# Kernel optimization log

Hardware: AMD Instinct MI355X
Metric: run time of the kernel (lower is better)

The kernel has to match this reference:

```python
import jax, jax.numpy as jnp
import numpy as np

N, K, C = 10000, 64, 128


def setup_inputs() -> dict:
    key = jax.random.key(0)
    ks = jax.random.split(key, 6)
    return {
        "real": jax.random.normal(ks[0], (N, C), dtype=jnp.float32),
        "imag": jax.random.normal(ks[1], (N, C), dtype=jnp.float32),
        "Qreal": jax.random.normal(ks[2], (N, K), dtype=jnp.float32) / np.sqrt(N),
        "Qimag": jax.random.normal(ks[3], (N, K), dtype=jnp.float32) / np.sqrt(N),
        "Ritz": jax.random.uniform(ks[4], (K,), dtype=jnp.float32),
        "weight": jax.random.normal(ks[5], (C, C), dtype=jnp.float32) * np.sqrt(2.0 / (C + C)),  # xavier-ish scale
        "long_diff": 5,
    }


def reference(real, imag, Qreal, Qimag, Ritz, weight, long_diff):
    # TT = Ritz ** long_diff ; spectral filters L = Q diag(TT) Q^H split into real/imag
    TT = jnp.power(Ritz, long_diff)  # [K]
    QrT = Qreal * TT  # [N,K] columns scaled by TT (== Qreal @ diag(TT))
    QiT = Qimag * TT
    L_real = QrT @ Qreal.T + QiT @ Qimag.T  # [N,N]
    L_imag = QiT @ Qreal.T - QrT @ Qimag.T  # [N,N]
    # complex spmm + shared dense weight: (L @ X_complex) @ W
    res_real = (L_real @ real - L_imag @ imag) @ weight  # [N,C]
    res_imag = (L_imag @ real + L_real @ imag) @ weight  # [N,C]
    # complex ReLU: mask by sign of real part
    mask = (res_real >= 0).astype(res_real.dtype)
    return real + mask * res_real, imag + mask * res_imag
```

## Files before the change

kernel.cpp:

```cpp
#include <hip/hip_runtime.h>

#define NN 10000
#define KK 64
#define CC 128
#define OUTOFF (NN * CC)
#define NA 256
#define CHUNKS_A 625

__device__ __forceinline__ float4 f4fma(float s, float4 v, float4 a) {
    a.x = fmaf(s, v.x, a.x); a.y = fmaf(s, v.y, a.y);
    a.z = fmaf(s, v.z, a.z); a.w = fmaf(s, v.w, a.w);
    return a;
}
__device__ __forceinline__ float4 f4add(float4 a, float4 b) {
    a.x += b.x; a.y += b.y; a.z += b.z; a.w += b.w; return a;
}


__global__ __launch_bounds__(512) void kA(const float* __restrict__ re,
                                          const float* __restrict__ im,
                                          const float* __restrict__ Qr,
                                          const float* __restrict__ Qi,
                                          float* __restrict__ part)
{
    __shared__ float4 smem[1536];
    const int t = threadIdx.x;
    const int bid = blockIdx.x;
    const int kt = t & 15;
    const int ctA = t >> 4;
    const int row_q = (t & 255) >> 4, q_q = t & 15;
    const int row_x = t >> 5,          q_x = t & 31;
    const float4* gq  = (const float4*)((t < 256) ? Qr : Qi);
    const float4* gre = (const float4*)re;
    const float4* gim = (const float4*)im;

    float aU[4][4] = {}, aV[4][4] = {};

    int cb = bid;
    float4 r0 = gq [(size_t)(cb * 16 + row_q) * 16 + q_q];
    float4 r1 = gre[(size_t)(cb * 16 + row_x) * 32 + q_x];
    float4 r2 = gim[(size_t)(cb * 16 + row_x) * 32 + q_x];

    while (true) {
        smem[t] = r0; smem[512 + t] = r1; smem[1024 + t] = r2;
        __syncthreads();
        const int nx = cb + NA;
        if (nx < CHUNKS_A) {
            const int m0 = nx * 16;
            r0 = gq [(size_t)(m0 + row_q) * 16 + q_q];
            r1 = gre[(size_t)(m0 + row_x) * 32 + q_x];
            r2 = gim[(size_t)(m0 + row_x) * 32 + q_x];
        }
#pragma unroll 4
        for (int rr = 0; rr < 16; ++rr) {
            float4 q_r = smem[rr * 16 + kt];
            float4 q_i = smem[256 + rr * 16 + kt];
            float4 x_r = smem[512 + rr * 32 + ctA];
            float4 x_i = smem[1024 + rr * 32 + ctA];
            float qr_[4] = {q_r.x, q_r.y, q_r.z, q_r.w};
            float qi_[4] = {q_i.x, q_i.y, q_i.z, q_i.w};
            float xr_[4] = {x_r.x, x_r.y, x_r.z, x_r.w};
            float xi_[4] = {x_i.x, x_i.y, x_i.z, x_i.w};
#pragma unroll
            for (int a = 0; a < 4; ++a)
#pragma unroll
                for (int b = 0; b < 4; ++b) {
                    aU[a][b] = fmaf(qr_[a], xr_[b], aU[a][b]);
                    aU[a][b] = fmaf(qi_[a], xi_[b], aU[a][b]);
                    aV[a][b] = fmaf(qi_[a], xr_[b], aV[a][b]);
                    aV[a][b] = fmaf(-qr_[a], xi_[b], aV[a][b]);
                }
        }
        __syncthreads();
        if (nx >= CHUNKS_A) break;
        cb = nx;
    }
    float* base = part + (size_t)bid * 16384;
    const int k0 = kt * 4, c0 = ctA * 4;
#pragma unroll
    for (int a = 0; a < 4; ++a) {
        *(float4*)(base + (k0 + a) * CC + c0)        = make_float4(aU[a][0], aU[a][1], aU[a][2], aU[a][3]);
        *(float4*)(base + 8192 + (k0 + a) * CC + c0) = make_float4(aV[a][0], aV[a][1], aV[a][2], aV[a][3]);
    }
}

__global__ __launch_bounds__(256) void kRB(const float* __restrict__ part,
                                           const float* __restrict__ Ritz,
                                           const int* __restrict__ ldp,
                                           const float* __restrict__ W,
                                           float* __restrict__ UVW)
{
    __shared__ float4 red4[256];
    __shared__ float rowS[128];
    const int t = threadIdx.x;
    const int m = blockIdx.x >> 6, k = blockIdx.x & 63;
    const int q = t & 31, sl = t >> 5;

    const float4* p = (const float4*)part + (size_t)sl * 4096 + m * 2048 + k * 32 + q;
    float4 z = make_float4(0.f, 0.f, 0.f, 0.f);
    float4 s0 = z, s1 = z, s2 = z, s3 = z;
#pragma unroll 2
    for (int jj = 0; jj < 8; ++jj) {
        s0 = f4add(s0, p[0]);
        s1 = f4add(s1, p[(size_t)8  * 4096]);
        s2 = f4add(s2, p[(size_t)16 * 4096]);
        s3 = f4add(s3, p[(size_t)24 * 4096]);
        p += (size_t)32 * 4096;
    }
    red4[t] = f4add(f4add(s0, s1), f4add(s2, s3));
    __syncthreads();
    if (t < 32) {
        float4 tot = z;
#pragma unroll
        for (int g = 0; g < 8; ++g) tot = f4add(tot, red4[g * 32 + t]);
        ((float4*)rowS)[t] = tot;
    }
    __syncthreads();
    if (t < 128) {
        float acc = 0.f;
#pragma unroll 8
        for (int cp = 0; cp < 128; ++cp)
            acc = fmaf(rowS[cp], W[cp * 128 + t], acc);
        const int ld = *ldp;
        const float rz = Ritz[k];
        float tt = 1.f;
        for (int i = 0; i < ld; ++i) tt *= rz;
        UVW[m * 8192 + k * 128 + t] = tt * acc;
    }
}

__global__ __launch_bounds__(256) void kC(const float* __restrict__ re,
                                          const float* __restrict__ im,
                                          const float* __restrict__ Qr,
                                          const float* __restrict__ Qi,
                                          const float* __restrict__ UVW,
                                          float* __restrict__ out)
{
    __shared__ float4 s[4096];
    const int t = threadIdx.x;
    {
        const float4* g = (const float4*)UVW;
        for (int i = t; i < 4096; i += 256) s[i] = g[i];
    }
    __syncthreads();
    const int ct = t & 31;
    const int r  = t >> 5;
    const int na = blockIdx.x * 16 + r;
    const int nb = na + 8;

    const float4* qra = (const float4*)(Qr + (size_t)na * KK);
    const float4* qia = (const float4*)(Qi + (size_t)na * KK);
    const float4* qrb = (const float4*)(Qr + (size_t)nb * KK);
    const float4* qib = (const float4*)(Qi + (size_t)nb * KK);

    float4 z = make_float4(0.f, 0.f, 0.f, 0.f);
    float4 Ra = z, Ia = z, Rb = z, Ib = z;

#pragma unroll 4
    for (int k4 = 0; k4 < 16; ++k4) {
        float4 QRa = qra[k4], QIa = qia[k4];
        float4 QRb = qrb[k4], QIb = qib[k4];
        float ar[4] = {QRa.x, QRa.y, QRa.z, QRa.w};
        float ai[4] = {QIa.x, QIa.y, QIa.z, QIa.w};
        float br[4] = {QRb.x, QRb.y, QRb.z, QRb.w};
        float bi[4] = {QIb.x, QIb.y, QIb.z, QIb.w};
#pragma unroll
        for (int j = 0; j < 4; ++j) {
            const int k = k4 * 4 + j;
            float4 uw = s[k * 32 + ct];
            float4 vw = s[2048 + k * 32 + ct];
            Ra = f4fma(ar[j], uw, Ra); Ra = f4fma(ai[j], vw, Ra);
            Ia = f4fma(ai[j], uw, Ia); Ia = f4fma(-ar[j], vw, Ia);
            Rb = f4fma(br[j], uw, Rb); Rb = f4fma(bi[j], vw, Rb);
            Ib = f4fma(bi[j], uw, Ib); Ib = f4fma(-br[j], vw, Ib);
        }
    }
    const int cc = ct * 4;
    {
        float4 rin = *(const float4*)(re + (size_t)na * CC + cc);
        float4 iin = *(const float4*)(im + (size_t)na * CC + cc);
        float4 orr, oii;
        orr.x = rin.x + (Ra.x >= 0.f ? Ra.x : 0.f); oii.x = iin.x + (Ra.x >= 0.f ? Ia.x : 0.f);
        orr.y = rin.y + (Ra.y >= 0.f ? Ra.y : 0.f); oii.y = iin.y + (Ra.y >= 0.f ? Ia.y : 0.f);
        orr.z = rin.z + (Ra.z >= 0.f ? Ra.z : 0.f); oii.z = iin.z + (Ra.z >= 0.f ? Ia.z : 0.f);
        orr.w = rin.w + (Ra.w >= 0.f ? Ra.w : 0.f); oii.w = iin.w + (Ra.w >= 0.f ? Ia.w : 0.f);
        *(float4*)(out + (size_t)na * CC + cc)          = orr;
        *(float4*)(out + OUTOFF + (size_t)na * CC + cc) = oii;
    }
    {
        float4 rin = *(const float4*)(re + (size_t)nb * CC + cc);
        float4 iin = *(const float4*)(im + (size_t)nb * CC + cc);
        float4 orr, oii;
        orr.x = rin.x + (Rb.x >= 0.f ? Rb.x : 0.f); oii.x = iin.x + (Rb.x >= 0.f ? Ib.x : 0.f);
        orr.y = rin.y + (Rb.y >= 0.f ? Rb.y : 0.f); oii.y = iin.y + (Rb.y >= 0.f ? Ib.y : 0.f);
        orr.z = rin.z + (Rb.z >= 0.f ? Rb.z : 0.f); oii.z = iin.z + (Rb.z >= 0.f ? Ib.z : 0.f);
        orr.w = rin.w + (Rb.w >= 0.f ? Rb.w : 0.f); oii.w = iin.w + (Rb.w >= 0.f ? Ib.w : 0.f);
        *(float4*)(out + (size_t)nb * CC + cc)          = orr;
        *(float4*)(out + OUTOFF + (size_t)nb * CC + cc) = oii;
    }
}

extern "C" void kernel_launch(void* const* d_in, const int* in_sizes, int n_in,
                              void* d_out, int out_size, void* d_ws, size_t ws_size,
                              hipStream_t stream) {
    const float* re   = (const float*)d_in[0];
    const float* im   = (const float*)d_in[1];
    const float* Qr   = (const float*)d_in[2];
    const float* Qi   = (const float*)d_in[3];
    const float* Ritz = (const float*)d_in[4];
    const float* W    = (const float*)d_in[5];
    const int*   ldp  = (const int*)d_in[6];
    float* out = (float*)d_out;
    float* ws  = (float*)d_ws;

    float* part = ws;
    float* UVW  = ws + (size_t)NA * 16384;

    kA <<<NA,  512, 0, stream>>>(re, im, Qr, Qi, part);
    kRB<<<128, 256, 0, stream>>>(part, Ritz, ldp, W, UVW);
    kC <<<625, 256, 0, stream>>>(re, im, Qr, Qi, UVW, out);
}
```

Baseline: 114.3 us.

## Fuse partial-sum reduction into first kernel via atomic ticket and grid spin-wait

The separate reduction kernel is merged into the first kernel. Each block takes an atomic ticket after writing its partials, and the last 128 ticket holders spin until all 256 blocks finish, then do the reduction plus weight multiply. This removes one kernel launch and its boundary gap, but adds a memset launch and relies on all 256 blocks being co-resident so the spin-wait cannot deadlock. The output kernel also moves to 512-thread blocks covering 32 rows each, with a tail guard.

After: 125.5 us. 9.8% more time.

```diff
diff --git a/kernel.cpp b/kernel.cpp
--- a/kernel.cpp
+++ b/kernel.cpp
@@ -6,6 +6,10 @@
 #define OUTOFF (NN * CC)
 #define NA 256
 #define CHUNKS_A 625
+#define NRED 128
+
+#define UVW_OFF ((size_t)NA * 16384)
+#define CNT_OFF (UVW_OFF + 16384)
 
 __device__ __forceinline__ float4 f4fma(float s, float4 v, float4 a) {
     a.x = fmaf(s, v.x, a.x); a.y = fmaf(s, v.y, a.y);
@@ -16,120 +20,135 @@
     a.x += b.x; a.y += b.y; a.z += b.z; a.w += b.w; return a;
 }
 
-
-__global__ __launch_bounds__(512) void kA(const float* __restrict__ re,
-                                          const float* __restrict__ im,
-                                          const float* __restrict__ Qr,
-                                          const float* __restrict__ Qi,
-                                          float* __restrict__ part)
+__global__ __launch_bounds__(512) void kAR(const float* __restrict__ re,
+                                           const float* __restrict__ im,
+                                           const float* __restrict__ Qr,
+                                           const float* __restrict__ Qi,
+                                           const float* __restrict__ Ritz,
+                                           const float* __restrict__ W,
+                                           const int* __restrict__ ldp,
+                                           float* __restrict__ ws)
 {
     __shared__ float4 smem[1536];
+    __shared__ int ticketS;
     const int t = threadIdx.x;
     const int bid = blockIdx.x;
-    const int kt = t & 15;
-    const int ctA = t >> 4;
-    const int row_q = (t & 255) >> 4, q_q = t & 15;
-    const int row_x = t >> 5,          q_x = t & 31;
-    const float4* gq  = (const float4*)((t < 256) ? Qr : Qi);
-    const float4* gre = (const float4*)re;
-    const float4* gim = (const float4*)im;
-
-    float aU[4][4] = {}, aV[4][4] = {};
-
-    int cb = bid;
-    float4 r0 = gq [(size_t)(cb * 16 + row_q) * 16 + q_q];
-    float4 r1 = gre[(size_t)(cb * 16 + row_x) * 32 + q_x];
-    float4 r2 = gim[(size_t)(cb * 16 + row_x) * 32 + q_x];
-
-    while (true) {
-        smem[t] = r0; smem[512 + t] = r1; smem[1024 + t] = r2;
+
+    {
+        const int kt = t & 15;
+        const int ctA = t >> 4;
+        const int row_q = (t & 255) >> 4, q_q = t & 15;
+        const int row_x = t >> 5,          q_x = t & 31;
+        const float4* gq  = (const float4*)((t < 256) ? Qr : Qi);
+        const float4* gre = (const float4*)re;
+        const float4* gim = (const float4*)im;
+
+        float aU[4][4] = {}, aV[4][4] = {};
+        int cb = bid;
+        float4 r0 = gq [(size_t)(cb * 16 + row_q) * 16 + q_q];
+        float4 r1 = gre[(size_t)(cb * 16 + row_x) * 32 + q_x];
+        float4 r2 = gim[(size_t)(cb * 16 + row_x) * 32 + q_x];
+
+        while (true) {
+            smem[t] = r0; smem[512 + t] = r1; smem[1024 + t] = r2;
+            __syncthreads();
+            const int nx = cb + NA;
+            if (nx < CHUNKS_A) {
+                const int m0 = nx * 16;
+                r0 = gq [(size_t)(m0 + row_q) * 16 + q_q];
+                r1 = gre[(size_t)(m0 + row_x) * 32 + q_x];
+                r2 = gim[(size_t)(m0 + row_x) * 32 + q_x];
+            }
+#pragma unroll 4
+            for (int rr = 0; rr < 16; ++rr) {
+                float4 q_r = smem[rr * 16 + kt];
+                float4 q_i = smem[256 + rr * 16 + kt];
+                float4 x_r = smem[512 + rr * 32 + ctA];
+                float4 x_i = smem[1024 + rr * 32 + ctA];
+                float qr_[4] = {q_r.x, q_r.y, q_r.z, q_r.w};
+                float qi_[4] = {q_i.x, q_i.y, q_i.z, q_i.w};
+                float xr_[4] = {x_r.x, x_r.y, x_r.z, x_r.w};
+                float xi_[4] = {x_i.x, x_i.y, x_i.z, x_i.w};
+#pragma unroll
+                for (int a = 0; a < 4; ++a)
+#pragma unroll
+                    for (int b = 0; b < 4; ++b) {
+                        aU[a][b] = fmaf(qr_[a], xr_[b], aU[a][b]);
+                        aU[a][b] = fmaf(qi_[a], xi_[b], aU[a][b]);
+                        aV[a][b] = fmaf(qi_[a], xr_[b], aV[a][b]);
+                        aV[a][b] = fmaf(-qr_[a], xi_[b], aV[a][b]);
+                    }
+            }
+            __syncthreads();
+            if (nx >= CHUNKS_A) break;
+            cb = nx;
+        }
+        float* base = ws + (size_t)bid * 16384;
+        const int k0 = kt * 4, c0 = ctA * 4;
+#pragma unroll
+        for (int a = 0; a < 4; ++a) {
+            *(float4*)(base + (k0 + a) * CC + c0)        = make_float4(aU[a][0], aU[a][1], aU[a][2], aU[a][3]);
+            *(float4*)(base + 8192 + (k0 + a) * CC + c0) = make_float4(aV[a][0], aV[a][1], aV[a][2], aV[a][3]);
+        }
+    }
+
+    unsigned* cnt = (unsigned*)(ws + CNT_OFF);
+    __syncthreads();
+    if (t == 0) {
+        __threadfence();
+        ticketS = (int)atomicAdd(cnt, 1u);
+    }
+    __syncthreads();
+    const int ticket = ticketS;
+    if (ticket < NA - NRED) return;
+    if (t == 0) {
+        while (__hip_atomic_load(cnt, __ATOMIC_RELAXED, __HIP_MEMORY_SCOPE_AGENT) < NA)
+            __builtin_amdgcn_s_sleep(2);
+        __threadfence();
+    }
+    __syncthreads();
+
+    {
+        const int role = ticket - (NA - NRED);
+        const int m = role >> 6, k = role & 63;
+        const int q = t & 31, sl = t >> 5;
+        const float4* part4 = (const float4*)ws;
+        const size_t base = (size_t)m * 2048 + k * 32 + q;
+        const float4 z = make_float4(0.f, 0.f, 0.f, 0.f);
+        float4 s0 = z, s1 = z, s2 = z, s3 = z;
+#pragma unroll
+        for (int jj = 0; jj < 4; ++jj) {
+            s0 = f4add(s0, part4[(size_t)(sl + 16 * (jj))      * 4096 + base]);
+            s1 = f4add(s1, part4[(size_t)(sl + 16 * (jj + 4))  * 4096 + base]);
+            s2 = f4add(s2, part4[(size_t)(sl + 16 * (jj + 8))  * 4096 + base]);
+            s3 = f4add(s3, part4[(size_t)(sl + 16 * (jj + 12)) * 4096 + base]);
+        }
+        float4* red4 = smem;
+        float*  rowS = (float*)(smem + 512);
+        red4[t] = f4add(f4add(s0, s1), f4add(s2, s3));
         __syncthreads();
-        const int nx = cb + NA;
-        if (nx < CHUNKS_A) {
-            const int m0 = nx * 16;
-            r0 = gq [(size_t)(m0 + row_q) * 16 + q_q];
-            r1 = gre[(size_t)(m0 + row_x) * 32 + q_x];
-            r2 = gim[(size_t)(m0 + row_x) * 32 + q_x];
-        }
-#pragma unroll 4
-        for (int rr = 0; rr < 16; ++rr) {
-            float4 q_r = smem[rr * 16 + kt];
-            float4 q_i = smem[256 + rr * 16 + kt];
-            float4 x_r = smem[512 + rr * 32 + ctA];
-            float4 x_i = smem[1024 + rr * 32 + ctA];
-            float qr_[4] = {q_r.x, q_r.y, q_r.z, q_r.w};
-            float qi_[4] = {q_i.x, q_i.y, q_i.z, q_i.w};
-            float xr_[4] = {x_r.x, x_r.y, x_r.z, x_r.w};
-            float xi_[4] = {x_i.x, x_i.y, x_i.z, x_i.w};
-#pragma unroll
-            for (int a = 0; a < 4; ++a)
-#pragma unroll
-                for (int b = 0; b < 4; ++b) {
-                    aU[a][b] = fmaf(qr_[a], xr_[b], aU[a][b]);
-                    aU[a][b] = fmaf(qi_[a], xi_[b], aU[a][b]);
-                    aV[a][b] = fmaf(qi_[a], xr_[b], aV[a][b]);
-                    aV[a][b] = fmaf(-qr_[a], xi_[b], aV[a][b]);
-                }
+        if (t < 32) {
+            float4 tot = z;
+#pragma unroll
+            for (int g = 0; g < 16; ++g) tot = f4add(tot, red4[g * 32 + t]);
+            ((float4*)rowS)[t] = tot;
         }
         __syncthreads();
-        if (nx >= CHUNKS_A) break;
-        cb = nx;
-    }
-    float* base = part + (size_t)bid * 16384;
-    const int k0 = kt * 4, c0 = ctA * 4;
-#pragma unroll
-    for (int a = 0; a < 4; ++a) {
-        *(float4*)(base + (k0 + a) * CC + c0)        = make_float4(aU[a][0], aU[a][1], aU[a][2], aU[a][3]);
-        *(float4*)(base + 8192 + (k0 + a) * CC + c0) = make_float4(aV[a][0], aV[a][1], aV[a][2], aV[a][3]);
-    }
-}
-
-__global__ __launch_bounds__(256) void kRB(const float* __restrict__ part,
-                                           const float* __restrict__ Ritz,
-                                           const int* __restrict__ ldp,
-                                           const float* __restrict__ W,
-                                           float* __restrict__ UVW)
-{
-    __shared__ float4 red4[256];
-    __shared__ float rowS[128];
-    const int t = threadIdx.x;
-    const int m = blockIdx.x >> 6, k = blockIdx.x & 63;
-    const int q = t & 31, sl = t >> 5;
-
-    const float4* p = (const float4*)part + (size_t)sl * 4096 + m * 2048 + k * 32 + q;
-    float4 z = make_float4(0.f, 0.f, 0.f, 0.f);
-    float4 s0 = z, s1 = z, s2 = z, s3 = z;
-#pragma unroll 2
-    for (int jj = 0; jj < 8; ++jj) {
-        s0 = f4add(s0, p[0]);
-        s1 = f4add(s1, p[(size_t)8  * 4096]);
-        s2 = f4add(s2, p[(size_t)16 * 4096]);
-        s3 = f4add(s3, p[(size_t)24 * 4096]);
-        p += (size_t)32 * 4096;
-    }
-    red4[t] = f4add(f4add(s0, s1), f4add(s2, s3));
-    __syncthreads();
-    if (t < 32) {
-        float4 tot = z;
-#pragma unroll
-        for (int g = 0; g < 8; ++g) tot = f4add(tot, red4[g * 32 + t]);
-        ((float4*)rowS)[t] = tot;
-    }
-    __syncthreads();
-    if (t < 128) {
-        float acc = 0.f;
+        if (t < 128) {
+            float acc = 0.f;
 #pragma unroll 8
-        for (int cp = 0; cp < 128; ++cp)
-            acc = fmaf(rowS[cp], W[cp * 128 + t], acc);
-        const int ld = *ldp;
-        const float rz = Ritz[k];
-        float tt = 1.f;
-        for (int i = 0; i < ld; ++i) tt *= rz;
-        UVW[m * 8192 + k * 128 + t] = tt * acc;
-    }
-}
-
-__global__ __launch_bounds__(256) void kC(const float* __restrict__ re,
+            for (int cp = 0; cp < 128; ++cp)
+                acc = fmaf(rowS[cp], W[cp * 128 + t], acc);
+            const int ld = *ldp;
+            const float rz = Ritz[k];
+            float tt = 1.f;
+            for (int i = 0; i < ld; ++i) tt *= rz;
+            (ws + UVW_OFF)[m * 8192 + k * 128 + t] = tt * acc;
+        }
+    }
+}
+
+__global__ __launch_bounds__(512) void kC(const float* __restrict__ re,
                                           const float* __restrict__ im,
                                           const float* __restrict__ Qr,
                                           const float* __restrict__ Qi,
@@ -140,18 +159,20 @@
     const int t = threadIdx.x;
     {
         const float4* g = (const float4*)UVW;
-        for (int i = t; i < 4096; i += 256) s[i] = g[i];
+        for (int i = t; i < 4096; i += 512) s[i] = g[i];
     }
     __syncthreads();
     const int ct = t & 31;
     const int r  = t >> 5;
-    const int na = blockIdx.x * 16 + r;
-    const int nb = na + 8;
+    const int na = blockIdx.x * 32 + r;
+    const int nb = na + 16;
+    const bool bok = (nb < NN);
+    const int nbs = bok ? nb : na;
 
     const float4* qra = (const float4*)(Qr + (size_t)na * KK);
     const float4* qia = (const float4*)(Qi + (size_t)na * KK);
-    const float4* qrb = (const float4*)(Qr + (size_t)nb * KK);
-    const float4* qib = (const float4*)(Qi + (size_t)nb * KK);
+    const float4* qrb = (const float4*)(Qr + (size_t)nbs * KK);
+    const float4* qib = (const float4*)(Qi + (size_t)nbs * KK);
 
     float4 z = make_float4(0.f, 0.f, 0.f, 0.f);
     float4 Ra = z, Ia = z, Rb = z, Ib = z;
@@ -165,14 +186,14 @@
         float br[4] = {QRb.x, QRb.y, QRb.z, QRb.w};
         float bi[4] = {QIb.x, QIb.y, QIb.z, QIb.w};
 #pragma unroll
-        for (int j = 0; j < 4; ++j) {
-            const int k = k4 * 4 + j;
+        for (int jj = 0; jj < 4; ++jj) {
+            const int k = k4 * 4 + jj;
             float4 uw = s[k * 32 + ct];
             float4 vw = s[2048 + k * 32 + ct];
-            Ra = f4fma(ar[j], uw, Ra); Ra = f4fma(ai[j], vw, Ra);
-            Ia = f4fma(ai[j], uw, Ia); Ia = f4fma(-ar[j], vw, Ia);
-            Rb = f4fma(br[j], uw, Rb); Rb = f4fma(bi[j], vw, Rb);
-            Ib = f4fma(bi[j], uw, Ib); Ib = f4fma(-br[j], vw, Ib);
+            Ra = f4fma(ar[jj], uw, Ra); Ra = f4fma(ai[jj], vw, Ra);
+            Ia = f4fma(ai[jj], uw, Ia); Ia = f4fma(-ar[jj], vw, Ia);
+            Rb = f4fma(br[jj], uw, Rb); Rb = f4fma(bi[jj], vw, Rb);
+            Ib = f4fma(bi[jj], uw, Ib); Ib = f4fma(-br[jj], vw, Ib);
         }
     }
     const int cc = ct * 4;
@@ -187,7 +208,7 @@
         *(float4*)(out + (size_t)na * CC + cc)          = orr;
         *(float4*)(out + OUTOFF + (size_t)na * CC + cc) = oii;
     }
-    {
+    if (bok) {
         float4 rin = *(const float4*)(re + (size_t)nb * CC + cc);
         float4 iin = *(const float4*)(im + (size_t)nb * CC + cc);
         float4 orr, oii;
@@ -213,10 +234,7 @@
     float* out = (float*)d_out;
     float* ws  = (float*)d_ws;
 
-    float* part = ws;
-    float* UVW  = ws + (size_t)NA * 16384;
-
-    kA <<<NA,  512, 0, stream>>>(re, im, Qr, Qi, part);
-    kRB<<<128, 256, 0, stream>>>(part, Ritz, ldp, W, UVW);
-    kC <<<625, 256, 0, stream>>>(re, im, Qr, Qi, UVW, out);
-}
+    hipMemsetAsync(ws + CNT_OFF, 0, 64, stream);
+    kAR<<<NA, 512, 0, stream>>>(re, im, Qr, Qi, Ritz, W, ldp, ws);
+    kC <<<313, 512, 0, stream>>>(re, im, Qr, Qi, ws + UVW_OFF, out);
+}
```
